# Optimization experiments

Hardware: AMD Instinct MI355X
Metric: run time of the kernel (lower is better)

The kernel has to match this reference:

```python
import jax, jax.numpy as jnp
import numpy as np

BATCH, SEQ, DIM = 8, 2048, 512
NUM_Q, CODEBOOK = 8, 1024


def setup_inputs() -> dict:
    key = jax.random.key(0)
    k1, k2 = jax.random.split(key)
    x = jax.random.normal(k1, (BATCH, SEQ, DIM), dtype=jnp.float32)
    # one codebook per quantizer (uniform codebook size -> stacked [q, c, d])
    codebooks = jax.random.normal(k2, (NUM_Q, CODEBOOK, DIM), dtype=jnp.float32)
    return {"x": x, "codebooks": codebooks}


def reference(x, codebooks):
    """Residual VQ (Algorithm 1, SoundStream). Sequential nearest-neighbor
    quantization of the residual with straight-through estimator.
    project_in/project_out are Identity (codebook_dim == dim).
    Returns (quantized_out [b,n,d], indices [b,n,q], commit_losses [q]).
    """
    residual = x
    quantized_out = jnp.zeros_like(x)
    all_indices = []
    all_losses = []
    num_q = codebooks.shape[0]
    for q in range(num_q):  # small fixed loop over quantizer layers
        cb = codebooks[q]  # [c, d]
        # argmin of squared euclidean distance; ||r||^2 is constant over codes
        scores = -2.0 * jnp.einsum('bnd,cd->bnc', residual, cb) \
                 + jnp.sum(cb * cb, axis=-1)  # [b, n, c]
        idx = jnp.argmin(scores, axis=-1)  # [b, n]
        quant = cb[idx]  # gather codes: [b, n, d]
        # commitment loss (mse of detached quantize vs layer input)
        commit = jnp.mean((jax.lax.stop_gradient(quant) - residual) ** 2)
        # straight-through estimator
        quant_st = residual + jax.lax.stop_gradient(quant - residual)
        quantized_out = quantized_out + quant_st
        residual = residual - jax.lax.stop_gradient(quant)
        all_indices.append(idx)
        all_losses.append(commit)
    indices = jnp.stack(all_indices, axis=-1)  # [b, n, q]
    losses = jnp.stack(all_losses)  # [q]
    return quantized_out, indices, losses
```

## Files before the change

kernel.cpp:

```cpp
#include <hip/hip_runtime.h>
#include <cstdint>
#include <cstddef>


#define BATCH 8
#define SEQ   2048
#define DIM   512
#define NUMQ  8
#define CODES 1024
#define NPTS  (BATCH*SEQ)
#define MPTS  64
#define NWG   (NPTS/MPTS)
#define NTHR  512
#define NCHUNK 32
#define CHUNK_BYTES 32768

#define OUT_IDX   (BATCH*SEQ*DIM)
#define OUT_LOSS  (OUT_IDX + BATCH*SEQ*NUMQ)

#define WS_LOSS   0
#define WS_CNORM  1024
#define WS_CBH    40960

typedef _Float16 f16x8  __attribute__((ext_vector_type(8)));
typedef _Float16 f16x4  __attribute__((ext_vector_type(4)));
typedef float    f32x16 __attribute__((ext_vector_type(16)));

__global__ void k_zero(double* loss) {
  if (threadIdx.x < NUMQ) loss[threadIdx.x] = 0.0;
}

__global__ void k_cnorm(const float* __restrict__ cb, float* __restrict__ cnorm) {
  int r = blockIdx.x * blockDim.x + threadIdx.x;
  const float* row = cb + (size_t)r * DIM;
  float s = 0.f;
  for (int d = 0; d < DIM; d += 4) {
    float4 v = *(const float4*)(row + d);
    s += v.x * v.x + v.y * v.y + v.z * v.z + v.w * v.w;
  }
  cnorm[r] = s;
}

__global__ void k_prep(const float* __restrict__ cb, unsigned char* __restrict__ cbH) {
  unsigned u = blockIdx.x * blockDim.x + threadIdx.x;
  unsigned h  = u & 1;
  unsigned v  = u >> 1;
  unsigned c  = v & 127;
  unsigned g  = (v >> 7) & 1;
  unsigned w  = (v >> 8) & 7;
  unsigned ks = (v >> 11) & 31;
  unsigned q  = v >> 16;
  unsigned code = (w << 7) | c;
  unsigned k = ks * 16 + g * 8 + h * 4;
  float4 val = *(const float4*)(cb + ((size_t)((q << 10) | code)) * DIM + k);
  f16x4 o;
  o[0] = (_Float16)val.x; o[1] = (_Float16)val.y;
  o[2] = (_Float16)val.z; o[3] = (_Float16)val.w;
  *(f16x4*)(cbH + (size_t)u * 8) = o;
}

struct BF { f16x8 b0, b1, b2, b3; };
__device__ __forceinline__ BF loadB(const unsigned char* __restrict__ p) {
  BF r;
  r.b0 = *(const f16x8*)(p);
  r.b1 = *(const f16x8*)(p + 512);
  r.b2 = *(const f16x8*)(p + 1024);
  r.b3 = *(const f16x8*)(p + 1536);
  return r;
}

__launch_bounds__(NTHR, 2)
__global__ void k_main(const float* __restrict__ x, const float* __restrict__ cb,
                       const unsigned char* __restrict__ cbH,
                       const float* __restrict__ cnorm,
                       double* __restrict__ lossAcc,
                       float* __restrict__ out)
{
  __shared__ __align__(16) unsigned char Af[MPTS * DIM * 2];
  __shared__ float          s1w[MPTS][8];
  __shared__ unsigned short id1w[MPTS][8];
  __shared__ unsigned short cand[MPTS][8][4];
  __shared__ unsigned char  ccnt[MPTS][8];
  __shared__ float          gmA[MPTS];
  __shared__ int            win0A[MPTS];
  __shared__ unsigned short idxs[MPTS][NUMQ];
  __shared__ double         lred[8];

  const int tid = threadIdx.x;
  const int cl  = tid & 63;
  const int w   = tid >> 6;
  const int l31 = cl & 31;
  const int l5  = cl >> 5;
  const int wg  = blockIdx.x;

  const int rp = tid >> 3;
  const int rj = tid & 7;
  const size_t gp = (size_t)wg * MPTS + rp;
  float4 r4[16];
  {
    const float4* xr = (const float4*)(x + gp * DIM + rj * 64);
    #pragma unroll
    for (int i = 0; i < 16; ++i) r4[i] = xr[i];
  }

  for (int q = 0; q < NUMQ; ++q) {
    const unsigned char* bq = cbH + ((size_t)q << 20) + (w << 12) + (l5 << 11) + (l31 << 4);

    BF s0 = loadB(bq);
    BF s1 = loadB(bq + CHUNK_BYTES);

    #pragma unroll
    for (int i = 0; i < 8; ++i) {
      float4 a = r4[2 * i], b = r4[2 * i + 1];
      f16x8 v;
      v[0] = (_Float16)a.x; v[1] = (_Float16)a.y; v[2] = (_Float16)a.z; v[3] = (_Float16)a.w;
      v[4] = (_Float16)b.x; v[5] = (_Float16)b.y; v[6] = (_Float16)b.z; v[7] = (_Float16)b.w;
      int sl = ((i << 3) | rj) ^ (rp & 31);
      *(f16x8*)(Af + rp * 1024 + (sl << 4)) = v;
    }
    __syncthreads();

    f32x16 acc[2][4];
    #pragma unroll
    for (int mt = 0; mt < 2; ++mt)
      #pragma unroll
      for (int nt = 0; nt < 4; ++nt)
        #pragma unroll
        for (int e = 0; e < 16; ++e) acc[mt][nt][e] = 0.0f;

    #pragma unroll 1
    for (int kk = 0; kk < 16; ++kk) {
      const int ks = kk << 1;
      {
        const int s5 = (ks << 1) | l5;
        const int sf = ((((s5 & 7) << 3) | (s5 >> 3)) ^ l31) << 4;
        f16x8 a0 = *(const f16x8*)(Af + l31 * 1024 + sf);
        f16x8 a1 = *(const f16x8*)(Af + 32768 + l31 * 1024 + sf);
        __builtin_amdgcn_s_setprio(1);
        acc[0][0] = __builtin_amdgcn_mfma_f32_32x32x16_f16(a0, s0.b0, acc[0][0], 0, 0, 0);
        acc[0][1] = __builtin_amdgcn_mfma_f32_32x32x16_f16(a0, s0.b1, acc[0][1], 0, 0, 0);
        acc[0][2] = __builtin_amdgcn_mfma_f32_32x32x16_f16(a0, s0.b2, acc[0][2], 0, 0, 0);
        acc[0][3] = __builtin_amdgcn_mfma_f32_32x32x16_f16(a0, s0.b3, acc[0][3], 0, 0, 0);
        acc[1][0] = __builtin_amdgcn_mfma_f32_32x32x16_f16(a1, s0.b0, acc[1][0], 0, 0, 0);
        acc[1][1] = __builtin_amdgcn_mfma_f32_32x32x16_f16(a1, s0.b1, acc[1][1], 0, 0, 0);
        acc[1][2] = __builtin_amdgcn_mfma_f32_32x32x16_f16(a1, s0.b2, acc[1][2], 0, 0, 0);
        acc[1][3] = __builtin_amdgcn_mfma_f32_32x32x16_f16(a1, s0.b3, acc[1][3], 0, 0, 0);
        __builtin_amdgcn_s_setprio(0);
        if (ks + 2 < NCHUNK) s0 = loadB(bq + (size_t)(ks + 2) * CHUNK_BYTES);
      }
      {
        const int ks1 = ks + 1;
        const int s5 = (ks1 << 1) | l5;
        const int sf = ((((s5 & 7) << 3) | (s5 >> 3)) ^ l31) << 4;
        f16x8 a0 = *(const f16x8*)(Af + l31 * 1024 + sf);
        f16x8 a1 = *(const f16x8*)(Af + 32768 + l31 * 1024 + sf);
        __builtin_amdgcn_s_setprio(1);
        acc[0][0] = __builtin_amdgcn_mfma_f32_32x32x16_f16(a0, s1.b0, acc[0][0], 0, 0, 0);
        acc[0][1] = __builtin_amdgcn_mfma_f32_32x32x16_f16(a0, s1.b1, acc[0][1], 0, 0, 0);
        acc[0][2] = __builtin_amdgcn_mfma_f32_32x32x16_f16(a0, s1.b2, acc[0][2], 0, 0, 0);
        acc[0][3] = __builtin_amdgcn_mfma_f32_32x32x16_f16(a0, s1.b3, acc[0][3], 0, 0, 0);
        acc[1][0] = __builtin_amdgcn_mfma_f32_32x32x16_f16(a1, s1.b0, acc[1][0], 0, 0, 0);
        acc[1][1] = __builtin_amdgcn_mfma_f32_32x32x16_f16(a1, s1.b1, acc[1][1], 0, 0, 0);
        acc[1][2] = __builtin_amdgcn_mfma_f32_32x32x16_f16(a1, s1.b2, acc[1][2], 0, 0, 0);
        acc[1][3] = __builtin_amdgcn_mfma_f32_32x32x16_f16(a1, s1.b3, acc[1][3], 0, 0, 0);
        __builtin_amdgcn_s_setprio(0);
        if (ks1 + 2 < NCHUNK) s1 = loadB(bq + (size_t)(ks1 + 2) * CHUNK_BYTES);
      }
    }

    {
      const float* cnq = cnorm + (q << 10) + (w << 7) + l31;
      const float cn0 = cnq[0], cn1 = cnq[32], cn2 = cnq[64], cn3 = cnq[96];
      #pragma unroll
      for (int mt = 0; mt < 2; ++mt) {
        acc[mt][0] = acc[mt][0] * -2.0f + cn0;
        acc[mt][1] = acc[mt][1] * -2.0f + cn1;
        acc[mt][2] = acc[mt][2] * -2.0f + cn2;
        acc[mt][3] = acc[mt][3] * -2.0f + cn3;
      }
    }

    #pragma unroll
    for (int mt = 0; mt < 2; ++mt)
      #pragma unroll
      for (int r = 0; r < 16; ++r) {
        float s = acc[mt][0][r]; int bi = l31;
        if (acc[mt][1][r] < s) { s = acc[mt][1][r]; bi = 32 + l31; }
        if (acc[mt][2][r] < s) { s = acc[mt][2][r]; bi = 64 + l31; }
        if (acc[mt][3][r] < s) { s = acc[mt][3][r]; bi = 96 + l31; }
        #pragma unroll
        for (int m = 1; m < 32; m <<= 1) {
          float os = __shfl_xor(s, m); int ob = __shfl_xor(bi, m);
          if (os < s || (os == s && ob < bi)) { s = os; bi = ob; }
        }
        if (l31 == 0) {
          int p = mt * 32 + (r & 3) + 8 * (r >> 2) + 4 * l5;
          s1w[p][w] = s; id1w[p][w] = (unsigned short)bi;
        }
      }
    __syncthreads();

    if (tid < MPTS) {
      int p = tid;
      float bs = s1w[p][0]; int bi = id1w[p][0];
      #pragma unroll
      for (int ww = 1; ww < 8; ++ww) {
        float s = s1w[p][ww];
        if (s < bs) { bs = s; bi = ww * 128 + id1w[p][ww]; }
      }
      gmA[p] = bs; win0A[p] = bi;
    }
    __syncthreads();

    #pragma unroll
    for (int mt = 0; mt < 2; ++mt)
      #pragma unroll
      for (int r = 0; r < 16; ++r) {
        const int p0 = mt * 32 + (r & 3) + 8 * (r >> 2);
        const float g0 = gmA[p0], g1 = gmA[p0 + 4];
        const float lim0 = g0 + 1.5f + 1e-4f * fabsf(g0);
        const float lim1 = g1 + 1.5f + 1e-4f * fabsf(g1);
        const float lim = l5 ? lim1 : lim0;
        unsigned long long b0 = __ballot(acc[mt][0][r] <= lim);
        unsigned long long b1 = __ballot(acc[mt][1][r] <= lim);
        unsigned long long b2 = __ballot(acc[mt][2][r] <= lim);
        unsigned long long b3 = __ballot(acc[mt][3][r] <= lim);
        if (cl == 0 || cl == 32) {
          const int p = p0 + (cl >> 3);
          unsigned short* cd = &cand[p][w][0];
          unsigned m0 = (cl == 0) ? (unsigned)b0 : (unsigned)(b0 >> 32);
          unsigned m1 = (cl == 0) ? (unsigned)b1 : (unsigned)(b1 >> 32);
          unsigned m2 = (cl == 0) ? (unsigned)b2 : (unsigned)(b2 >> 32);
          unsigned m3 = (cl == 0) ? (unsigned)b3 : (unsigned)(b3 >> 32);
          int n = 0;
          while (m0 && n < 4) { int bt = __builtin_ctz(m0); m0 &= m0 - 1; cd[n++] = (unsigned short)(bt); }
          while (m1 && n < 4) { int bt = __builtin_ctz(m1); m1 &= m1 - 1; cd[n++] = (unsigned short)(32 + bt); }
          while (m2 && n < 4) { int bt = __builtin_ctz(m2); m2 &= m2 - 1; cd[n++] = (unsigned short)(64 + bt); }
          while (m3 && n < 4) { int bt = __builtin_ctz(m3); m3 &= m3 - 1; cd[n++] = (unsigned short)(96 + bt); }
          ccnt[p][w] = (unsigned char)n;
        }
      }
    __syncthreads();

    #pragma unroll 1
    for (int pp = 0; pp < 8; ++pp) {
      const int p = (w << 3) + pp;
      int tot = 0;
      #pragma unroll
      for (int ww = 0; ww < 8; ++ww) tot += ccnt[p][ww];
      int winner;
      if (tot <= 1) {
        winner = win0A[p];
      } else {
        const size_t gpp = (size_t)wg * MPTS + p;
        double bs = 1.0e300, bs2 = 1.0e300; int bi = 0x7FFFFFFF;
        #pragma unroll 1
        for (int ww = 0; ww < 8; ++ww) {
          const int nn = ccnt[p][ww];
          #pragma unroll 1
          for (int si = 0; si < nn; ++si) {
            const int cc = ww * 128 + cand[p][ww][si];
            const float4* cr = (const float4*)(cb + ((size_t)q * CODES + cc) * DIM + (cl & 7) * 64);
            double dt = 0.0, cs = 0.0;
            #pragma unroll
            for (int i = 0; i < 16; ++i) {
              float4 cv = cr[i];
              dt += (double)r4[i].x * cv.x + (double)r4[i].y * cv.y
                  + (double)r4[i].z * cv.z + (double)r4[i].w * cv.w;
              cs += (double)cv.x * cv.x + (double)cv.y * cv.y
                  + (double)cv.z * cv.z + (double)cv.w * cv.w;
            }
            #pragma unroll
            for (int m = 1; m < 8; m <<= 1) { dt += __shfl_xor(dt, m); cs += __shfl_xor(cs, m); }
            double dtb = __shfl(dt, pp * 8), csb = __shfl(cs, pp * 8);
            double s = -2.0 * dtb + csb;
            if (s < bs) { bs2 = bs; bs = s; bi = cc; }
            else if (s < bs2) { bs2 = s; }
          }
        }
        if (bs2 - bs <= 1e-3 + 1e-6 * fabs(bs)) {
          bs = 1.0e300; bi = 0x7FFFFFFF;
          const float4* xr2 = (const float4*)(x + gpp * DIM + (cl & 7) * 64);
          #pragma unroll 1
          for (int ww = 0; ww < 8; ++ww) {
            const int nn = ccnt[p][ww];
            #pragma unroll 1
            for (int si = 0; si < nn; ++si) {
              const int cc = ww * 128 + cand[p][ww][si];
              const float4* cr = (const float4*)(cb + ((size_t)q * CODES + cc) * DIM + (cl & 7) * 64);
              double dt = 0.0, cs = 0.0;
              #pragma unroll 1
              for (int i = 0; i < 16; ++i) {
                float4 xv = xr2[i];
                double rhx = xv.x, rhy = xv.y, rhz = xv.z, rhw = xv.w;
                #pragma unroll 1
                for (int t2 = 0; t2 < q; ++t2) {
                  const float4* qr = (const float4*)(cb + ((size_t)t2 * CODES + idxs[p][t2]) * DIM + (cl & 7) * 64);
                  float4 qv = qr[i];
                  rhx -= (double)qv.x; rhy -= (double)qv.y;
                  rhz -= (double)qv.z; rhw -= (double)qv.w;
                }
                float4 cv = cr[i];
                dt += rhx * cv.x + rhy * cv.y + rhz * cv.z + rhw * cv.w;
                cs += (double)cv.x * cv.x + (double)cv.y * cv.y
                    + (double)cv.z * cv.z + (double)cv.w * cv.w;
              }
              #pragma unroll
              for (int m = 1; m < 8; m <<= 1) { dt += __shfl_xor(dt, m); cs += __shfl_xor(cs, m); }
              double dtb = __shfl(dt, pp * 8), csb = __shfl(cs, pp * 8);
              double s = -2.0 * dtb + csb;
              if (s < bs || (s == bs && cc < bi)) { bs = s; bi = cc; }
            }
          }
        }
        winner = bi;
      }
      if (cl == 0) idxs[p][q] = (unsigned short)winner;
    }
    __syncthreads();

    {
      const int win = idxs[rp][q];
      const float4* cr = (const float4*)(cb + ((size_t)q * CODES + win) * DIM + rj * 64);
      double ls = 0.0;
      #pragma unroll
      for (int i = 0; i < 16; ++i) {
        float4 cv = cr[i];
        float dx = cv.x - r4[i].x, dy = cv.y - r4[i].y;
        float dz = cv.z - r4[i].z, dw = cv.w - r4[i].w;
        ls += (double)dx * dx + (double)dy * dy + (double)dz * dz + (double)dw * dw;
        r4[i].x -= cv.x; r4[i].y -= cv.y; r4[i].z -= cv.z; r4[i].w -= cv.w;
      }
      #pragma unroll
      for (int m = 1; m < 64; m <<= 1) ls += __shfl_xor(ls, m);
      if (cl == 0) lred[w] = ls;
      __syncthreads();
      if (tid == 0) {
        double t = lred[0] + lred[1] + lred[2] + lred[3]
                 + lred[4] + lred[5] + lred[6] + lred[7];
        atomicAdd(lossAcc + q, t);
      }
      __syncthreads();
    }
  }

  {
    const float4* xr = (const float4*)(x + gp * DIM + rj * 64);
    float4* orow = (float4*)(out + gp * DIM + rj * 64);
    #pragma unroll
    for (int i = 0; i < 16; ++i) {
      float4 xv = xr[i];
      float4 o;
      o.x = xv.x - r4[i].x; o.y = xv.y - r4[i].y;
      o.z = xv.z - r4[i].z; o.w = xv.w - r4[i].w;
      orow[i] = o;
    }
  }
  if (tid < MPTS) {
    float* ob = out + OUT_IDX + ((size_t)wg * MPTS + tid) * NUMQ;
    #pragma unroll
    for (int j = 0; j < NUMQ; ++j) ob[j] = (float)idxs[tid][j];
  }
}

__global__ void k_fin(const double* __restrict__ loss, float* __restrict__ out) {
  int t = threadIdx.x;
  if (t < NUMQ)
    out[OUT_LOSS + t] = (float)(loss[t] / (double)((size_t)BATCH * SEQ * DIM));
}

extern "C" void kernel_launch(void* const* d_in, const int* in_sizes, int n_in,
                              void* d_out, int out_size, void* d_ws, size_t ws_size,
                              hipStream_t stream) {
  (void)in_sizes; (void)n_in; (void)out_size; (void)ws_size;
  const float* x  = (const float*)d_in[0];
  const float* cb = (const float*)d_in[1];
  float* out = (float*)d_out;
  char* ws = (char*)d_ws;
  double* loss = (double*)(ws + WS_LOSS);
  float* cnorm = (float*)(ws + WS_CNORM);
  unsigned char* cbH = (unsigned char*)(ws + WS_CBH);

  k_zero<<<1, 64, 0, stream>>>(loss);
  k_cnorm<<<NUMQ * CODES / 256, 256, 0, stream>>>(cb, cnorm);
  k_prep<<<NUMQ * NCHUNK * CHUNK_BYTES / 8 / 256, 256, 0, stream>>>(cb, cbH);
  k_main<<<NWG, NTHR, 0, stream>>>(x, cb, cbH, cnorm, loss, out);
  k_fin<<<1, 64, 0, stream>>>(loss, out);
}
```

Measured before the change: 613.1 us.

## Parallelize candidate refinement across points per wave and precompute double code norms

The fp64 candidate re-scoring now handles 8 points at once per wave, one per 8-lane group, instead of looping over points serially. Code norms in double precision are precomputed by a new kernel, so the per-candidate norm sum is no longer recomputed. The per-row argmin now uses an fminf shuffle reduction plus a ballot to pick the lowest index instead of shuffling score/index pairs. Dot-product and loss accumulations are split into several independent chains. The cost is warp divergence when candidate counts differ between the groups, plus one extra small prep kernel.

After: 543.1 us. 11.4% less time.

```diff
diff --git a/kernel.cpp b/kernel.cpp
--- a/kernel.cpp
+++ b/kernel.cpp
@@ -21,6 +21,7 @@
 #define WS_LOSS   0
 #define WS_CNORM  1024
 #define WS_CBH    40960
+#define WS_CNORMD (WS_CBH + NUMQ*NCHUNK*CHUNK_BYTES)
 
 typedef _Float16 f16x8  __attribute__((ext_vector_type(8)));
 typedef _Float16 f16x4  __attribute__((ext_vector_type(4)));
@@ -39,6 +40,20 @@
     s += v.x * v.x + v.y * v.y + v.z * v.z + v.w * v.w;
   }
   cnorm[r] = s;
+}
+
+__global__ void k_cnormd(const float* __restrict__ cb, double* __restrict__ cnd) {
+  int r = blockIdx.x * blockDim.x + threadIdx.x;
+  const float4* row = (const float4*)(cb + (size_t)r * DIM);
+  double d0 = 0, d1 = 0, d2 = 0, d3 = 0;
+  for (int i = 0; i < 128; i += 4) {
+    float4 a = row[i], b = row[i + 1], c = row[i + 2], d = row[i + 3];
+    d0 += (double)a.x * a.x + (double)a.y * a.y + (double)a.z * a.z + (double)a.w * a.w;
+    d1 += (double)b.x * b.x + (double)b.y * b.y + (double)b.z * b.z + (double)b.w * b.w;
+    d2 += (double)c.x * c.x + (double)c.y * c.y + (double)c.z * c.z + (double)c.w * c.w;
+    d3 += (double)d.x * d.x + (double)d.y * d.y + (double)d.z * d.z + (double)d.w * d.w;
+  }
+  cnd[r] = (d0 + d1) + (d2 + d3);
 }
 
 __global__ void k_prep(const float* __restrict__ cb, unsigned char* __restrict__ cbH) {
@@ -73,6 +88,7 @@
 __global__ void k_main(const float* __restrict__ x, const float* __restrict__ cb,
                        const unsigned char* __restrict__ cbH,
                        const float* __restrict__ cnorm,
+                       const double* __restrict__ cnormd,
                        double* __restrict__ lossAcc,
                        float* __restrict__ out)
 {
@@ -188,14 +204,16 @@
         if (acc[mt][1][r] < s) { s = acc[mt][1][r]; bi = 32 + l31; }
         if (acc[mt][2][r] < s) { s = acc[mt][2][r]; bi = 64 + l31; }
         if (acc[mt][3][r] < s) { s = acc[mt][3][r]; bi = 96 + l31; }
+        float smin = s;
         #pragma unroll
-        for (int m = 1; m < 32; m <<= 1) {
-          float os = __shfl_xor(s, m); int ob = __shfl_xor(bi, m);
-          if (os < s || (os == s && ob < bi)) { s = os; bi = ob; }
-        }
+        for (int m = 1; m < 32; m <<= 1) smin = fminf(smin, __shfl_xor(smin, m));
+        unsigned long long bm = __ballot(s == smin);
+        unsigned half = l5 ? (unsigned)(bm >> 32) : (unsigned)bm;
+        int first = __builtin_ctz(half) + (l5 << 5);
+        int id = __shfl(bi, first);
         if (l31 == 0) {
           int p = mt * 32 + (r & 3) + 8 * (r >> 2) + 4 * l5;
-          s1w[p][w] = s; id1w[p][w] = (unsigned short)bi;
+          s1w[p][w] = smin; id1w[p][w] = (unsigned short)id;
         }
       }
     __syncthreads();
@@ -242,95 +260,109 @@
       }
     __syncthreads();
 
-    #pragma unroll 1
-    for (int pp = 0; pp < 8; ++pp) {
-      const int p = (w << 3) + pp;
+    {
+      const int g  = cl >> 3;
+      const int gl = cl & 7;
+      const int p  = (w << 3) + g;
       int tot = 0;
       #pragma unroll
       for (int ww = 0; ww < 8; ++ww) tot += ccnt[p][ww];
-      int winner;
-      if (tot <= 1) {
-        winner = win0A[p];
-      } else {
-        const size_t gpp = (size_t)wg * MPTS + p;
+      int winner = win0A[p];
+      int mtot = tot;
+      #pragma unroll
+      for (int m = 1; m < 64; m <<= 1) { int o = __shfl_xor(mtot, m); if (o > mtot) mtot = o; }
+      if (mtot > 1) {
+        const size_t gpp = gp;
         double bs = 1.0e300, bs2 = 1.0e300; int bi = 0x7FFFFFFF;
         #pragma unroll 1
-        for (int ww = 0; ww < 8; ++ww) {
-          const int nn = ccnt[p][ww];
-          #pragma unroll 1
-          for (int si = 0; si < nn; ++si) {
-            const int cc = ww * 128 + cand[p][ww][si];
-            const float4* cr = (const float4*)(cb + ((size_t)q * CODES + cc) * DIM + (cl & 7) * 64);
-            double dt = 0.0, cs = 0.0;
+        for (int k = 0; k < mtot; ++k) {
+          int cc = -1;
+          if (tot > 1 && k < tot) {
+            int rem = k, ww = 0;
+            #pragma unroll 1
+            for (; ww < 7; ++ww) { int nn = ccnt[p][ww]; if (rem < nn) break; rem -= nn; }
+            cc = ww * 128 + cand[p][ww][rem];
+          }
+          double dt = 0.0;
+          if (cc >= 0) {
+            const float4* cr = (const float4*)(cb + ((size_t)q * CODES + cc) * DIM + gl * 64);
+            double d0 = 0, d1 = 0, d2 = 0, d3 = 0;
             #pragma unroll
-            for (int i = 0; i < 16; ++i) {
-              float4 cv = cr[i];
-              dt += (double)r4[i].x * cv.x + (double)r4[i].y * cv.y
-                  + (double)r4[i].z * cv.z + (double)r4[i].w * cv.w;
-              cs += (double)cv.x * cv.x + (double)cv.y * cv.y
-                  + (double)cv.z * cv.z + (double)cv.w * cv.w;
+            for (int i = 0; i < 16; i += 4) {
+              float4 c0 = cr[i], c1 = cr[i + 1], c2 = cr[i + 2], c3 = cr[i + 3];
+              d0 += (double)r4[i].x * c0.x + (double)r4[i].y * c0.y
+                  + (double)r4[i].z * c0.z + (double)r4[i].w * c0.w;
+              d1 += (double)r4[i + 1].x * c1.x + (double)r4[i + 1].y * c1.y
+                  + (double)r4[i + 1].z * c1.z + (double)r4[i + 1].w * c1.w;
+              d2 += (double)r4[i + 2].x * c2.x + (double)r4[i + 2].y * c2.y
+                  + (double)r4[i + 2].z * c2.z + (double)r4[i + 2].w * c2.w;
+              d3 += (double)r4[i + 3].x * c3.x + (double)r4[i + 3].y * c3.y
+                  + (double)r4[i + 3].z * c3.z + (double)r4[i + 3].w * c3.w;
             }
-            #pragma unroll
-            for (int m = 1; m < 8; m <<= 1) { dt += __shfl_xor(dt, m); cs += __shfl_xor(cs, m); }
-            double dtb = __shfl(dt, pp * 8), csb = __shfl(cs, pp * 8);
-            double s = -2.0 * dtb + csb;
+            dt = (d0 + d1) + (d2 + d3);
+          }
+          #pragma unroll
+          for (int m = 1; m < 8; m <<= 1) dt += __shfl_xor(dt, m);
+          if (cc >= 0) {
+            double s = -2.0 * dt + cnormd[(q << 10) + cc];
             if (s < bs) { bs2 = bs; bs = s; bi = cc; }
             else if (s < bs2) { bs2 = s; }
           }
         }
-        if (bs2 - bs <= 1e-3 + 1e-6 * fabs(bs)) {
+        if (tot > 1 && bs2 - bs <= 1e-3 + 1e-6 * fabs(bs)) {
           bs = 1.0e300; bi = 0x7FFFFFFF;
-          const float4* xr2 = (const float4*)(x + gpp * DIM + (cl & 7) * 64);
+          const float4* xr2 = (const float4*)(x + gpp * DIM + gl * 64);
           #pragma unroll 1
-          for (int ww = 0; ww < 8; ++ww) {
-            const int nn = ccnt[p][ww];
+          for (int k = 0; k < tot; ++k) {
+            int rem = k, ww = 0;
             #pragma unroll 1
-            for (int si = 0; si < nn; ++si) {
-              const int cc = ww * 128 + cand[p][ww][si];
-              const float4* cr = (const float4*)(cb + ((size_t)q * CODES + cc) * DIM + (cl & 7) * 64);
-              double dt = 0.0, cs = 0.0;
+            for (; ww < 7; ++ww) { int nn = ccnt[p][ww]; if (rem < nn) break; rem -= nn; }
+            const int cc = ww * 128 + cand[p][ww][rem];
+            const float4* cr = (const float4*)(cb + ((size_t)q * CODES + cc) * DIM + gl * 64);
+            double dt = 0.0;
+            #pragma unroll 1
+            for (int i = 0; i < 16; ++i) {
+              float4 xv = xr2[i];
+              double rhx = xv.x, rhy = xv.y, rhz = xv.z, rhw = xv.w;
               #pragma unroll 1
-              for (int i = 0; i < 16; ++i) {
-                float4 xv = xr2[i];
-                double rhx = xv.x, rhy = xv.y, rhz = xv.z, rhw = xv.w;
-                #pragma unroll 1
-                for (int t2 = 0; t2 < q; ++t2) {
-                  const float4* qr = (const float4*)(cb + ((size_t)t2 * CODES + idxs[p][t2]) * DIM + (cl & 7) * 64);
-                  float4 qv = qr[i];
-                  rhx -= (double)qv.x; rhy -= (double)qv.y;
-                  rhz -= (double)qv.z; rhw -= (double)qv.w;
-                }
-                float4 cv = cr[i];
-                dt += rhx * cv.x + rhy * cv.y + rhz * cv.z + rhw * cv.w;
-                cs += (double)cv.x * cv.x + (double)cv.y * cv.y
-                    + (double)cv.z * cv.z + (double)cv.w * cv.w;
+              for (int t2 = 0; t2 < q; ++t2) {
+                const float4* qr = (const float4*)(cb + ((size_t)t2 * CODES + idxs[p][t2]) * DIM + gl * 64);
+                float4 qv = qr[i];
+                rhx -= (double)qv.x; rhy -= (double)qv.y;
+                rhz -= (double)qv.z; rhw -= (double)qv.w;
               }
-              #pragma unroll
-              for (int m = 1; m < 8; m <<= 1) { dt += __shfl_xor(dt, m); cs += __shfl_xor(cs, m); }
-              double dtb = __shfl(dt, pp * 8), csb = __shfl(cs, pp * 8);
-              double s = -2.0 * dtb + csb;
-              if (s < bs || (s == bs && cc < bi)) { bs = s; bi = cc; }
+              float4 cv = cr[i];
+              dt += rhx * cv.x + rhy * cv.y + rhz * cv.z + rhw * cv.w;
             }
+            #pragma unroll
+            for (int m = 1; m < 8; m <<= 1) dt += __shfl_xor(dt, m);
+            double s = -2.0 * dt + cnormd[(q << 10) + cc];
+            if (s < bs || (s == bs && cc < bi)) { bs = s; bi = cc; }
           }
         }
-        winner = bi;
-      }
-      if (cl == 0) idxs[p][q] = (unsigned short)winner;
+        if (tot > 1) winner = bi;
+      }
+      if (gl == 0) idxs[p][q] = (unsigned short)winner;
     }
     __syncthreads();
 
     {
       const int win = idxs[rp][q];
       const float4* cr = (const float4*)(cb + ((size_t)q * CODES + win) * DIM + rj * 64);
-      double ls = 0.0;
-      #pragma unroll
-      for (int i = 0; i < 16; ++i) {
-        float4 cv = cr[i];
-        float dx = cv.x - r4[i].x, dy = cv.y - r4[i].y;
-        float dz = cv.z - r4[i].z, dw = cv.w - r4[i].w;
-        ls += (double)dx * dx + (double)dy * dy + (double)dz * dz + (double)dw * dw;
-        r4[i].x -= cv.x; r4[i].y -= cv.y; r4[i].z -= cv.z; r4[i].w -= cv.w;
-      }
+      double ls0 = 0.0, ls1 = 0.0;
+      #pragma unroll
+      for (int i = 0; i < 16; i += 2) {
+        float4 c0 = cr[i], c1 = cr[i + 1];
+        float dx0 = c0.x - r4[i].x, dy0 = c0.y - r4[i].y;
+        float dz0 = c0.z - r4[i].z, dw0 = c0.w - r4[i].w;
+        ls0 += (double)dx0 * dx0 + (double)dy0 * dy0 + (double)dz0 * dz0 + (double)dw0 * dw0;
+        r4[i].x -= c0.x; r4[i].y -= c0.y; r4[i].z -= c0.z; r4[i].w -= c0.w;
+        float dx1 = c1.x - r4[i + 1].x, dy1 = c1.y - r4[i + 1].y;
+        float dz1 = c1.z - r4[i + 1].z, dw1 = c1.w - r4[i + 1].w;
+        ls1 += (double)dx1 * dx1 + (double)dy1 * dy1 + (double)dz1 * dz1 + (double)dw1 * dw1;
+        r4[i + 1].x -= c1.x; r4[i + 1].y -= c1.y; r4[i + 1].z -= c1.z; r4[i + 1].w -= c1.w;
+      }
+      double ls = ls0 + ls1;
       #pragma unroll
       for (int m = 1; m < 64; m <<= 1) ls += __shfl_xor(ls, m);
       if (cl == 0) lred[w] = ls;
@@ -380,10 +412,12 @@
   double* loss = (double*)(ws + WS_LOSS);
   float* cnorm = (float*)(ws + WS_CNORM);
   unsigned char* cbH = (unsigned char*)(ws + WS_CBH);
+  double* cnormd = (double*)(ws + WS_CNORMD);
 
   k_zero<<<1, 64, 0, stream>>>(loss);
   k_cnorm<<<NUMQ * CODES / 256, 256, 0, stream>>>(cb, cnorm);
+  k_cnormd<<<NUMQ * CODES / 256, 256, 0, stream>>>(cb, cnormd);
   k_prep<<<NUMQ * NCHUNK * CHUNK_BYTES / 8 / 256, 256, 0, stream>>>(cb, cbH);
-  k_main<<<NWG, NTHR, 0, stream>>>(x, cb, cbH, cnorm, loss, out);
+  k_main<<<NWG, NTHR, 0, stream>>>(x, cb, cbH, cnorm, cnormd, loss, out);
   k_fin<<<1, 64, 0, stream>>>(loss, out);
 }
```
